# Kernel optimization log

Measured on AMD Instinct MI355X. Metric: run time of the kernel, lower is better.

Reference implementation:

```python
import jax, jax.numpy as jnp
import numpy as np

K = 20
EPS = 1e-5
SLOPE = 0.2


def setup_inputs() -> dict:
    key = jax.random.key(0)
    k1, k2 = jax.random.split(key, 2)
    B, C, N, O = 2, 64, 8192, 64
    x = jax.random.normal(k1, (B, C, N), dtype=jnp.float32)
    W = jax.random.normal(k2, (O, 2 * C), dtype=jnp.float32) * 0.05  # Conv2d 1x1, bias=False
    gamma = jnp.ones((O,), dtype=jnp.float32)
    beta = jnp.zeros((O,), dtype=jnp.float32)
    return {"x": x, "W": W, "gamma": gamma, "beta": beta}


def reference(x, W, gamma, beta):
    # x: (B, C, N)
    B, C, N = x.shape
    xt = jnp.swapaxes(x, 1, 2)  # (B, N, C)

    # --- get_GraphFeatures: KNN by negative squared euclidean distance ---
    inner = jnp.einsum('bnc,bmc->bnm', xt, xt)          # (B, N, N)
    sq = jnp.sum(xt * xt, axis=-1)                      # (B, N)
    neg_dist = 2.0 * inner - sq[:, :, None] - sq[:, None, :]
    _, idx = jax.lax.top_k(neg_dist, K)                 # (B, N, K) int32

    # gather neighbor features: (B, N, K, C)
    nbr = jax.vmap(lambda pts, i: pts[i])(xt, idx)
    center = xt[:, :, None, :]                          # (B, N, 1, C)
    # edge feature: concat(x_j - x_i, x_i) -> (B, N, K, 2C)
    edge = jnp.concatenate([nbr - center, jnp.broadcast_to(center, nbr.shape)], axis=-1)

    # --- 1x1 conv (pointwise GEMM) -> (B, O, N, K) ---
    h = jnp.einsum('bnkf,of->bonk', edge, W)

    # --- BatchNorm2d (training-mode batch stats over B, N, K per channel) ---
    mean = jnp.mean(h, axis=(0, 2, 3), keepdims=True)
    var = jnp.var(h, axis=(0, 2, 3), keepdims=True)
    h = (h - mean) * jax.lax.rsqrt(var + EPS)
    h = h * gamma[None, :, None, None] + beta[None, :, None, None]

    # --- LeakyReLU(0.2) + max over neighbors ---
    h = jnp.where(h >= 0, h, SLOPE * h)
    return jnp.max(h, axis=-1)                          # (B, O, N)
```

## Files before the change

kernel.cpp:

```cpp
#include <hip/hip_runtime.h>
#include <cfloat>

#define BB 2
#define NN 8192
#define OO 64
#define KK 20
#define QB 128
#define MS 8
#define CHUNK 1024
#define CAPQ 192
#define RB 9
#define RBS 10

using f16x8  = __attribute__((ext_vector_type(8))) _Float16;
using f32x16 = __attribute__((ext_vector_type(16))) float;
typedef unsigned long long u64;

#define XH_OFF ((size_t)0)
#define XL_OFF (XH_OFF + (size_t)BB*NN*32)
#define SQ_OFF (XL_OFF + (size_t)BB*NN*32)
#define Y1_OFF (SQ_OFF + (size_t)BB*NN)
#define Y2_OFF (Y1_OFF + (size_t)BB*NN*64)
#define TH_OFF (Y2_OFF + (size_t)BB*NN*64)
#define CN_OFF (TH_OFF + (size_t)BB*NN)
#define TL_OFF (CN_OFF + (size_t)BB*NN)
#define CA_OFF (TL_OFF + (size_t)2*BB*NN*KK)
#define IX_OFF (CA_OFF + (size_t)BB*NN*CAPQ*2)
#define HX_OFF (IX_OFF + (size_t)BB*NN*KK)
#define HN_OFF (HX_OFF + (size_t)BB*NN*64)
#define ST_OFF (HN_OFF + (size_t)BB*NN*64)

__device__ __forceinline__ size_t frag_off(int b, int tile, int t, int lane) {
    return ((((size_t)b * (NN / 32) + tile) * 4 + t) * 64 + lane) * 8;
}

__device__ __forceinline__ unsigned fmap(float f) {
    unsigned u = __float_as_uint(f);
    return (u & 0x80000000u) ? ~u : (u | 0x80000000u);
}

__device__ __forceinline__ void sort16(float* v) {
#pragma unroll
    for (int k = 2; k <= 16; k <<= 1) {
#pragma unroll
        for (int j = k >> 1; j > 0; j >>= 1) {
#pragma unroll
            for (int i = 0; i < 16; ++i) {
                int l = i ^ j;
                if (l > i) {
                    bool up = ((i & k) == 0);
                    float mn = fminf(v[i], v[l]);
                    float mx = fmaxf(v[i], v[l]);
                    v[i] = up ? mn : mx;
                    v[l] = up ? mx : mn;
                }
            }
        }
    }
}
__device__ __forceinline__ void bmerge32(float* A) {
#pragma unroll
    for (int j = 16; j > 0; j >>= 1) {
#pragma unroll
        for (int i = 0; i < 32; ++i) {
            if ((i & j) == 0) {
                float mn = fminf(A[i], A[i | j]);
                float mx = fmaxf(A[i], A[i | j]);
                A[i] = mn;
                A[i | j] = mx;
            }
        }
    }
}
__device__ __forceinline__ void merge32_16(float* A, const float* B) {
#pragma unroll
    for (int i = 16; i < 32; ++i) A[i] = fminf(A[i], B[31 - i]);
    bmerge32(A);
}
__device__ __forceinline__ void merge32_32(float* A, const float* B) {
    float t[32];
#pragma unroll
    for (int i = 0; i < 32; ++i) t[i] = fminf(A[i], B[31 - i]);
    bmerge32(t);
#pragma unroll
    for (int i = 0; i < 32; ++i) A[i] = t[i];
}

__device__ __forceinline__ void load_atile(const _Float16* __restrict__ xh,
                                           const _Float16* __restrict__ xl,
                                           int b, int ptile, int lane,
                                           f16x8* Ah, f16x8* Al) {
#pragma unroll
    for (int t = 0; t < 4; ++t) {
        size_t o = frag_off(b, ptile, t, lane);
        Ah[t] = *(const f16x8*)&xh[o];
        Al[t] = *(const f16x8*)&xl[o];
    }
}

__device__ __forceinline__ void dist_from_frags(const f16x8* Ah, const f16x8* Al,
                                                const float* sqs, int sbase, int kh,
                                                const f16x8* Qh, const f16x8* Ql,
                                                float* dv) {
    f32x16 c0, c1;
#pragma unroll
    for (int i = 0; i < 16; ++i) { c0[i] = 0.f; c1[i] = 0.f; }
#pragma unroll
    for (int t = 0; t < 4; ++t) {
        c0 = __builtin_amdgcn_mfma_f32_32x32x16_f16(Ah[t], Qh[t], c0, 0, 0, 0);
        c1 = __builtin_amdgcn_mfma_f32_32x32x16_f16(Ah[t], Ql[t], c1, 0, 0, 0);
        c1 = __builtin_amdgcn_mfma_f32_32x32x16_f16(Al[t], Qh[t], c1, 0, 0, 0);
    }
#pragma unroll
    for (int r2 = 0; r2 < 4; ++r2) {
        float4 sv = *(const float4*)&sqs[sbase + 8 * r2 + 4 * kh];
        float svv[4] = {sv.x, sv.y, sv.z, sv.w};
#pragma unroll
        for (int j = 0; j < 4; ++j) {
            int i = r2 * 4 + j;
            float d = fmaf(-2.f, c0[i], svv[j]);
            dv[i] = fmaf(-9.765625e-4f, c1[i], d);
        }
    }
}

__device__ __forceinline__ void load_qfrag(const _Float16* __restrict__ xh,
                                           const _Float16* __restrict__ xl,
                                           int b, int qbase, int lane,
                                           f16x8* Qh, f16x8* Ql) {
    const int qtile = qbase >> 5;
#pragma unroll
    for (int t = 0; t < 4; ++t) {
        size_t o = frag_off(b, qtile, t, lane);
        Qh[t] = *(const f16x8*)&xh[o];
        Ql[t] = *(const f16x8*)&xl[o];
    }
}

__global__ void __launch_bounds__(256, 2)
kA(const float* __restrict__ x, const float* __restrict__ W,
   float* __restrict__ ws) {
    __shared__ __align__(16) float w1s[32 * 64];
    __shared__ __align__(16) float w2s[32 * 64];
    __shared__ float xs[64 * 65];
    __shared__ float tb[64 * 33];
    const int bb = blockIdx.z;
    const int og = blockIdx.y;
    const int obase = og * 32;
    const int nbase = blockIdx.x * 64;
    const int tn = threadIdx.x & 63, tq = threadIdx.x >> 6;

    for (int i = threadIdx.x; i < 2048; i += 256) {
        int ol = i >> 6, c = i & 63;
        float a = W[(obase + ol) * 128 + c];
        float d = W[(obase + ol) * 128 + 64 + c];
        w1s[i] = a;
        w2s[i] = d - a;
    }
    for (int i = threadIdx.x; i < 4096; i += 256) {
        int c = i >> 6, nl = i & 63;
        xs[c * 65 + nl] = x[((size_t)bb * 64 + c) * NN + nbase + nl];
    }
    if (og == 0) {
        if (blockIdx.x == 0 && bb == 0 && threadIdx.x < 128)
            ws[ST_OFF + threadIdx.x] = 0.f;
        int gid = (bb * 128 + blockIdx.x) * 256 + threadIdx.x;
        if (gid < BB * NN) ((int*)(ws + CN_OFF))[gid] = 0;
    }
    __syncthreads();

    float xc[64];
#pragma unroll
    for (int c = 0; c < 64; ++c) xc[c] = xs[c * 65 + tn];

    if (og == 0 && tq == 0) {
        float sqv = 0.f;
#pragma unroll
        for (int c = 0; c < 64; ++c) sqv = fmaf(xc[c], xc[c], sqv);
        int n = nbase + tn;
        ws[SQ_OFF + (size_t)bb * NN + n] = sqv;
        _Float16* xh = (_Float16*)(ws + XH_OFF);
        _Float16* xl = (_Float16*)(ws + XL_OFF);
        int tile = n >> 5, r = n & 31;
#pragma unroll
        for (int t = 0; t < 4; ++t) {
#pragma unroll
            for (int kh = 0; kh < 2; ++kh) {
                f16x8 vh, vl;
#pragma unroll
                for (int j = 0; j < 8; ++j) {
                    float v = xc[t * 16 + kh * 8 + j];
                    _Float16 h = (_Float16)v;
                    vh[j] = h;
                    vl[j] = (_Float16)((v - (float)h) * 2048.f);
                }
                size_t o = frag_off(bb, tile, t, kh * 32 + r);
                *(f16x8*)&xh[o] = vh;
                *(f16x8*)&xl[o] = vl;
            }
        }
    }

    float a1v[8], a2v[8];
#pragma unroll
    for (int o2 = 0; o2 < 8; ++o2) {
        int ol = tq * 8 + o2;
        const float4* w1v = (const float4*)&w1s[ol * 64];
        const float4* w2v = (const float4*)&w2s[ol * 64];
        float a1 = 0.f, a2 = 0.f;
#pragma unroll
        for (int c4 = 0; c4 < 16; ++c4) {
            float4 v1 = w1v[c4];
            float4 v2 = w2v[c4];
            a1 = fmaf(v1.x, xc[4*c4],   a1);
            a1 = fmaf(v1.y, xc[4*c4+1], a1);
            a1 = fmaf(v1.z, xc[4*c4+2], a1);
            a1 = fmaf(v1.w, xc[4*c4+3], a1);
            a2 = fmaf(v2.x, xc[4*c4],   a2);
            a2 = fmaf(v2.y, xc[4*c4+1], a2);
            a2 = fmaf(v2.z, xc[4*c4+2], a2);
            a2 = fmaf(v2.w, xc[4*c4+3], a2);
        }
        a1v[o2] = a1;
        a2v[o2] = a2;
    }

    const int lo = threadIdx.x & 31;
    const int lp = (threadIdx.x >> 5) & 1;
#pragma unroll
    for (int o2 = 0; o2 < 8; ++o2)
        tb[tn * 33 + tq * 8 + o2] = a1v[o2];
    __syncthreads();
#pragma unroll
    for (int j = 0; j < 8; ++j) {
        int r = tq * 16 + 2 * j + lp;
        ws[Y1_OFF + ((size_t)bb * NN + nbase + r) * 64 + obase + lo] = tb[r * 33 + lo];
    }
    __syncthreads();
#pragma unroll
    for (int o2 = 0; o2 < 8; ++o2)
        tb[tn * 33 + tq * 8 + o2] = a2v[o2];
    __syncthreads();
#pragma unroll
    for (int j = 0; j < 8; ++j) {
        int r = tq * 16 + 2 * j + lp;
        ws[Y2_OFF + ((size_t)bb * NN + nbase + r) * 64 + obase + lo] = tb[r * 33 + lo];
    }
}

__global__ void __launch_bounds__(256, 3)
kT(const _Float16* __restrict__ xh, const _Float16* __restrict__ xl,
   const float* __restrict__ sq, float* __restrict__ thrL) {
    __shared__ float mrg[32 * 128];
    __shared__ __align__(16) float sqs[1024];
    const int tid  = threadIdx.x;
    const int lane = tid & 63;
    const int wv   = tid >> 6;
    const int qcol = lane & 31;
    const int kh   = lane >> 5;
    const int b     = blockIdx.y >> 1;
    const int s     = blockIdx.y & 1;
    const int qbase = blockIdx.x * 32;

    for (int i = tid; i < 1024; i += 256)
        sqs[i] = sq[(size_t)b * NN + s * 1024 + i];

    f16x8 Qh[4], Ql[4];
    load_qfrag(xh, xl, b, qbase, lane, Qh, Ql);
    __syncthreads();

    float dk[32];
#pragma unroll
    for (int i = 0; i < 32; ++i) dk[i] = FLT_MAX;

    const int p0 = s * 1024 + wv * 256;
    for (int pt = p0; pt < p0 + 256; pt += 32) {
        f16x8 Ah[4], Al[4];
        load_atile(xh, xl, b, pt >> 5, lane, Ah, Al);
        float dv[16];
        dist_from_frags(Ah, Al, sqs, pt - s * 1024, kh, Qh, Ql, dv);
        float m16 = dv[0];
#pragma unroll
        for (int i = 1; i < 16; ++i) m16 = fminf(m16, dv[i]);
        if (__any(m16 < dk[KK - 1])) {
            sort16(dv);
            merge32_16(dk, dv);
        }
    }

    {
        float B[32];
#pragma unroll
        for (int j = 0; j < 32; ++j) B[j] = __shfl(dk[j], lane | 32);
        merge32_32(dk, B);
    }
    if (kh == 0) {
#pragma unroll
        for (int j = 0; j < 32; ++j) mrg[j * 128 + wv * 32 + qcol] = dk[j];
    }
    __syncthreads();

    if (tid < 32) {
        float B[32];
#pragma unroll 1
        for (int w = 1; w < 4; ++w) {
#pragma unroll
            for (int j = 0; j < 32; ++j) B[j] = mrg[j * 128 + w * 32 + tid];
            merge32_32(dk, B);
        }
        size_t base = (((size_t)b * 2 + s) * NN + qbase + tid) * KK;
#pragma unroll
        for (int j = 0; j < KK; ++j) thrL[base + j] = dk[j];
    }
}

__global__ void kM2(const float* __restrict__ thrL, float* __restrict__ thr) {
    int gid = blockIdx.x * 256 + threadIdx.x;
    int b = gid >> 13, q = gid & (NN - 1);
    const float* A = &thrL[(((size_t)b * 2 + 0) * NN + q) * KK];
    const float* B = &thrL[(((size_t)b * 2 + 1) * NN + q) * KK];
    int ia = 0, ib = 0;
    float v = 0.f;
#pragma unroll
    for (int t = 0; t < KK; ++t) {
        float av = A[ia], bv = B[ib];
        bool ta = av <= bv;
        v = ta ? av : bv;
        ia += ta ? 1 : 0;
        ib += ta ? 0 : 1;
    }
    thr[gid] = v + fabsf(v) * 1e-6f + 1e-6f;
}

__global__ void __launch_bounds__(256, 4)
kS(const _Float16* __restrict__ xh, const _Float16* __restrict__ xl,
   const float* __restrict__ sq, const float* __restrict__ thr,
   int* __restrict__ cnt, u64* __restrict__ cand) {
    __shared__ __align__(16) char tbuf[2][8192];
    __shared__ u64 lbuf[256 * RBS];
    __shared__ __align__(16) float sqs[CHUNK];
    const int tid  = threadIdx.x;
    const int lane = tid & 63;
    const int wv   = tid >> 6;
    const int qcol = lane & 31;
    const int kh   = lane >> 5;
    const int id     = blockIdx.x;
    const int ychunk = id & 7;
    const int qt     = (id >> 3) & 63;
    const int b      = (id >> 9) & 1;
    const int qbase  = qt * QB + wv * 32;
    const int pbase0 = ychunk * CHUNK;
    const int ptile0 = pbase0 >> 5;

    auto stage = [&](int ptile, char* buf) {
        const _Float16* gh = &xh[frag_off(b, ptile, wv, lane)];
        const _Float16* gl = &xl[frag_off(b, ptile, wv, lane)];
        __builtin_amdgcn_global_load_lds(
            (const __attribute__((address_space(1))) void*)gh,
            (__attribute__((address_space(3))) void*)(buf + wv * 1024), 16, 0, 0);
        __builtin_amdgcn_global_load_lds(
            (const __attribute__((address_space(1))) void*)gl,
            (__attribute__((address_space(3))) void*)(buf + 4096 + wv * 1024), 16, 0, 0);
    };

    for (int i = tid; i < CHUNK; i += 256)
        sqs[i] = sq[(size_t)b * NN + pbase0 + i];

    f16x8 Qh[4], Ql[4];
    load_qfrag(xh, xl, b, qbase, lane, Qh, Ql);

    const size_t qidx = (size_t)b * NN + qbase + qcol;
    const float tv = thr[qidx];
    const size_t cb = qidx * CAPQ;
    int c_ = 0;

    stage(ptile0, tbuf[0]);
    __syncthreads();

    auto flushS = [&]() {
        if (c_ > 0) {
            int base = atomicAdd(&cnt[qidx], c_);
#pragma unroll 1
            for (int j = 0; j < c_; ++j) {
                int slot = base + j;
                if (slot < CAPQ) cand[cb + slot] = lbuf[tid * RBS + j];
            }
            c_ = 0;
        }
    };

#pragma unroll 1
    for (int tt = 0; tt < CHUNK / 32; ++tt) {
        if (tt + 1 < CHUNK / 32)
            stage(ptile0 + tt + 1, tbuf[(tt + 1) & 1]);

        const char* cbuf = tbuf[tt & 1];
        f16x8 Ah[4], Al[4];
#pragma unroll
        for (int t = 0; t < 4; ++t) {
            Ah[t] = *(const f16x8*)(cbuf + t * 1024 + lane * 16);
            Al[t] = *(const f16x8*)(cbuf + 4096 + t * 1024 + lane * 16);
        }
        float dv[16];
        dist_from_frags(Ah, Al, sqs, tt * 32, kh, Qh, Ql, dv);

        const int pb4 = pbase0 + tt * 32 + 4 * kh;
#pragma unroll
        for (int i = 0; i < 16; ++i) {
            float d = dv[i];
            if (d <= tv) {
                int id2 = pb4 + ((i & 3) + 8 * (i >> 2));
                lbuf[tid * RBS + c_] = ((u64)fmap(d) << 32) | (unsigned)id2;
                if (++c_ == RB) flushS();
            }
        }
        __syncthreads();
    }
    flushS();
}

__global__ void __launch_bounds__(64)
kP(const int* __restrict__ cnt, const u64* __restrict__ cand,
   int* __restrict__ idxK) {
    const int lane = threadIdx.x;
    const int qloc = lane & 31;
    const int par  = lane >> 5;
    const int q = blockIdx.x * 32 + qloc;
    int m = cnt[q];
    m = m < CAPQ ? m : CAPQ;
    const int nj = (m - par + 1) >> 1;
    u64 kk[KK];
#pragma unroll
    for (int i = 0; i < KK; ++i) kk[i] = ~0ull;

    auto insU = [&](u64 v) {
        kk[KK - 1] = v;
#pragma unroll
        for (int i = KK - 1; i > 0; --i) {
            u64 a = kk[i - 1], c = kk[i];
            bool sw = c < a;
            kk[i - 1] = sw ? c : a;
            kk[i]     = sw ? a : c;
        }
    };

    const u64* cp = &cand[(size_t)q * CAPQ + par];
#pragma unroll 1
    for (int j = 0; j < CAPQ / 2; ++j) {
        if (!__any(j < nj)) break;
        u64 v = cp[2 * j];
        if ((j < nj) && v < kk[KK - 1]) insU(v);
    }

#pragma unroll
    for (int j = 0; j < KK; ++j) {
        u64 v = __shfl(kk[j], lane | 32);
        bool ins = (par == 0) && v < kk[KK - 1];
        if (!__any(ins)) break;
        if (ins) insU(v);
    }

    if (par == 0) {
        int* op = &idxK[(size_t)q * KK];
#pragma unroll
        for (int i = 0; i < KK; ++i) op[i] = (int)(unsigned)(kk[i] & 0xffffffffu);
    }
}

__global__ void kC1(const float* __restrict__ y1, const float* __restrict__ y2,
                    const int* __restrict__ idxK, float* __restrict__ hmaxT,
                    float* __restrict__ hminT, float* __restrict__ stats) {
    __shared__ int li[32 * KK];
    __shared__ float red[256];
    __shared__ float thm[32 * 65];
    __shared__ float thn[32 * 65];
    int b = blockIdx.y;
    int o = threadIdx.x & 63;
    int nn = threadIdx.x >> 6;
    int nbase = blockIdx.x * 32;

    for (int i = threadIdx.x; i < 32 * KK; i += 256)
        li[i] = idxK[((size_t)b * NN + nbase) * KK + i];
    __syncthreads();

    float s = 0.f, ss = 0.f;
    for (int gidx = 0; gidx < 8; ++gidx) {
        int nl = gidx * 4 + nn;
        int n = nbase + nl;
        float y2v = y2[((size_t)b * NN + n) * 64 + o];
        float hm = -FLT_MAX, hn = FLT_MAX;
        const int* lin = &li[nl * KK];
#pragma unroll 4
        for (int k = 0; k < KK; ++k) {
            int j = lin[k];
            float h = y1[((size_t)b * NN + j) * 64 + o] + y2v;
            s += h;
            ss += h * h;
            hm = fmaxf(hm, h);
            hn = fminf(hn, h);
        }
        thm[nl * 65 + o] = hm;
        thn[nl * 65 + o] = hn;
    }
    __syncthreads();

    int l = threadIdx.x & 31, g = threadIdx.x >> 5;
#pragma unroll
    for (int i = 0; i < 8; ++i) {
        int o2 = g * 8 + i;
        hmaxT[((size_t)b * 64 + o2) * NN + nbase + l] = thm[l * 65 + o2];
        hminT[((size_t)b * 64 + o2) * NN + nbase + l] = thn[l * 65 + o2];
    }

    __syncthreads();
    red[threadIdx.x] = s;
    __syncthreads();
    if (threadIdx.x < 64) {
        float v = red[o] + red[64 + o] + red[128 + o] + red[192 + o];
        atomicAdd(&stats[o], v);
    }
    __syncthreads();
    red[threadIdx.x] = ss;
    __syncthreads();
    if (threadIdx.x < 64) {
        float v = red[o] + red[64 + o] + red[128 + o] + red[192 + o];
        atomicAdd(&stats[64 + o], v);
    }
}

__global__ void kC3(const float* __restrict__ hmaxT, const float* __restrict__ hminT,
                    const float* __restrict__ stats, const float* __restrict__ gamma,
                    const float* __restrict__ beta, float* __restrict__ out) {
    int o = blockIdx.x;
    int half = blockIdx.y;
    int b = blockIdx.z;
    const float c = (float)BB * NN * KK;
    float mean = stats[o] / c;
    float var = stats[64 + o] / c - mean * mean;
    float rs = rsqrtf(var + 1e-5f);
    float a = gamma[o] * rs;
    float b2 = beta[o] - a * mean;
    size_t rowb = ((size_t)b * 64 + o) * NN;
    int n0 = half * (NN / 2), n1 = n0 + NN / 2;
    for (int n = n0 + threadIdx.x; n < n1; n += 256) {
        float hm = hmaxT[rowb + n];
        float hn = hminT[rowb + n];
        float hs = (a >= 0.f) ? hm : hn;
        float v = a * hs + b2;
        v = (v >= 0.f) ? v : 0.2f * v;
        out[rowb + n] = v;
    }
}

extern "C" void kernel_launch(void* const* d_in, const int* in_sizes, int n_in,
                              void* d_out, int out_size, void* d_ws, size_t ws_size,
                              hipStream_t stream) {
    const float* x     = (const float*)d_in[0];
    const float* W     = (const float*)d_in[1];
    const float* gamma = (const float*)d_in[2];
    const float* beta  = (const float*)d_in[3];
    float* out = (float*)d_out;
    float* ws  = (float*)d_ws;

    _Float16* xh = (_Float16*)(ws + XH_OFF);
    _Float16* xl = (_Float16*)(ws + XL_OFF);
    float* sq    = ws + SQ_OFF;
    float* y1    = ws + Y1_OFF;
    float* y2    = ws + Y2_OFF;
    float* thr   = ws + TH_OFF;
    int*   cnt   = (int*)(ws + CN_OFF);
    float* thrL  = ws + TL_OFF;
    u64*   cand  = (u64*)(ws + CA_OFF);
    int*   idxK  = (int*)(ws + IX_OFF);
    float* hmaxT = ws + HX_OFF;
    float* hminT = ws + HN_OFF;
    float* stats = ws + ST_OFF;

    kA<<<dim3(NN / 64, 2, BB), 256, 0, stream>>>(x, W, ws);
    kT<<<dim3(NN / 32, 2 * BB), 256, 0, stream>>>(xh, xl, sq, thrL);
    kM2<<<dim3(BB * NN / 256), 256, 0, stream>>>(thrL, thr);
    kS<<<dim3(MS * (NN / QB) * BB), 256, 0, stream>>>(xh, xl, sq, thr, cnt, cand);
    kP<<<dim3(BB * NN / 32), 64, 0, stream>>>(cnt, cand, idxK);
    kC1<<<dim3(NN / 32, BB), 256, 0, stream>>>(y1, y2, idxK, hmaxT, hminT, stats);
    kC3<<<dim3(OO, 2, BB), 256, 0, stream>>>(hmaxT, hminT, stats, gamma, beta, out);
}
```

Before: 281.5 us.

## Parallelize candidate selection 4-way, vectorize threshold merge, batch gather loads

kM2 now loads each pair of sorted 20-element lists with float4 loads and finds the 20th smallest through a branch-free min/max formula instead of a serial merge with dependent loads. kP assigns four lanes to each query instead of two, unrolls the candidate loop by two, and combines the per-lane top-K lists with a two-level butterfly merge. kC1 issues all 20 neighbor gathers before reducing, to overlap memory latency, and gets launch bounds. The trade-off is more registers per thread and extra merge steps in kP.

```diff
diff --git a/kernel.cpp b/kernel.cpp
--- a/kernel.cpp
+++ b/kernel.cpp
@@ -317,18 +317,20 @@
 __global__ void kM2(const float* __restrict__ thrL, float* __restrict__ thr) {
     int gid = blockIdx.x * 256 + threadIdx.x;
     int b = gid >> 13, q = gid & (NN - 1);
-    const float* A = &thrL[(((size_t)b * 2 + 0) * NN + q) * KK];
-    const float* B = &thrL[(((size_t)b * 2 + 1) * NN + q) * KK];
-    int ia = 0, ib = 0;
-    float v = 0.f;
-#pragma unroll
-    for (int t = 0; t < KK; ++t) {
-        float av = A[ia], bv = B[ib];
-        bool ta = av <= bv;
-        v = ta ? av : bv;
-        ia += ta ? 1 : 0;
-        ib += ta ? 0 : 1;
-    }
+    float A[KK], Bv[KK];
+    const float4* pa = (const float4*)&thrL[(((size_t)b * 2 + 0) * NN + q) * KK];
+    const float4* pb = (const float4*)&thrL[(((size_t)b * 2 + 1) * NN + q) * KK];
+#pragma unroll
+    for (int i = 0; i < 5; ++i) {
+        float4 va = pa[i];
+        float4 vb = pb[i];
+        A[4*i] = va.x;  A[4*i+1] = va.y;  A[4*i+2] = va.z;  A[4*i+3] = va.w;
+        Bv[4*i] = vb.x; Bv[4*i+1] = vb.y; Bv[4*i+2] = vb.z; Bv[4*i+3] = vb.w;
+    }
+    float v = fminf(Bv[KK - 1], A[KK - 1]);
+#pragma unroll
+    for (int i = 1; i < KK; ++i)
+        v = fminf(v, fmaxf(A[i - 1], Bv[KK - 1 - i]));
     thr[gid] = v + fabsf(v) * 1e-6f + 1e-6f;
 }
 
@@ -419,16 +421,23 @@
     flushS();
 }
 
-__global__ void __launch_bounds__(64)
+__global__ void __launch_bounds__(256)
 kP(const int* __restrict__ cnt, const u64* __restrict__ cand,
    int* __restrict__ idxK) {
-    const int lane = threadIdx.x;
-    const int qloc = lane & 31;
-    const int par  = lane >> 5;
-    const int q = blockIdx.x * 32 + qloc;
+    const int tid  = threadIdx.x;
+    const int par  = tid & 3;
+    const int q = blockIdx.x * 64 + (tid >> 2);
     int m = cnt[q];
     m = m < CAPQ ? m : CAPQ;
-    const int nj = (m - par + 1) >> 1;
+    const int nj = (m - par + 3) >> 2;
+
+    int njW = nj;
+#pragma unroll
+    for (int s2 = 32; s2 >= 1; s2 >>= 1) {
+        int o = __shfl_xor(njW, s2);
+        njW = njW > o ? njW : o;
+    }
+
     u64 kk[KK];
 #pragma unroll
     for (int i = 0; i < KK; ++i) kk[i] = ~0ull;
@@ -446,18 +455,27 @@
 
     const u64* cp = &cand[(size_t)q * CAPQ + par];
 #pragma unroll 1
-    for (int j = 0; j < CAPQ / 2; ++j) {
-        if (!__any(j < nj)) break;
-        u64 v = cp[2 * j];
-        if ((j < nj) && v < kk[KK - 1]) insU(v);
-    }
-
-#pragma unroll
-    for (int j = 0; j < KK; ++j) {
-        u64 v = __shfl(kk[j], lane | 32);
-        bool ins = (par == 0) && v < kk[KK - 1];
-        if (!__any(ins)) break;
-        if (ins) insU(v);
+    for (int j = 0; j < njW; j += 2) {
+        u64 v0 = cp[4 * j];
+        u64 v1 = cp[4 * (j + 1)];
+        bool i0 = (j < nj) && v0 < kk[KK - 1];
+        bool i1 = (j + 1 < nj) && v1 < kk[KK - 1];
+        if (__any(i0 || i1)) {
+            if (i0) insU(v0);
+            if (i1 && v1 < kk[KK - 1]) insU(v1);
+        }
+    }
+
+#pragma unroll
+    for (int s2 = 2; s2 >= 1; s2 >>= 1) {
+        bool absorb = (par & s2) == 0;
+#pragma unroll 1
+        for (int j = 0; j < KK; ++j) {
+            u64 v = __shfl_xor(kk[j], s2);
+            bool ins = absorb && v < kk[KK - 1];
+            if (!__any(ins)) break;
+            if (ins) insU(v);
+        }
     }
 
     if (par == 0) {
@@ -467,9 +485,10 @@
     }
 }
 
-__global__ void kC1(const float* __restrict__ y1, const float* __restrict__ y2,
-                    const int* __restrict__ idxK, float* __restrict__ hmaxT,
-                    float* __restrict__ hminT, float* __restrict__ stats) {
+__global__ void __launch_bounds__(256, 2)
+kC1(const float* __restrict__ y1, const float* __restrict__ y2,
+    const int* __restrict__ idxK, float* __restrict__ hmaxT,
+    float* __restrict__ hminT, float* __restrict__ stats) {
     __shared__ int li[32 * KK];
     __shared__ float red[256];
     __shared__ float thm[32 * 65];
@@ -488,12 +507,17 @@
         int nl = gidx * 4 + nn;
         int n = nbase + nl;
         float y2v = y2[((size_t)b * NN + n) * 64 + o];
-        float hm = -FLT_MAX, hn = FLT_MAX;
         const int* lin = &li[nl * KK];
-#pragma unroll 4
+        float hv[KK];
+#pragma unroll
         for (int k = 0; k < KK; ++k) {
             int j = lin[k];
-            float h = y1[((size_t)b * NN + j) * 64 + o] + y2v;
+            hv[k] = y1[((size_t)b * NN + j) * 64 + o];
+        }
+        float hm = -FLT_MAX, hn = FLT_MAX;
+#pragma unroll
+        for (int k = 0; k < KK; ++k) {
+            float h = hv[k] + y2v;
             s += h;
             ss += h * h;
             hm = fmaxf(hm, h);
@@ -580,7 +604,7 @@
     kT<<<dim3(NN / 32, 2 * BB), 256, 0, stream>>>(xh, xl, sq, thrL);
     kM2<<<dim3(BB * NN / 256), 256, 0, stream>>>(thrL, thr);
     kS<<<dim3(MS * (NN / QB) * BB), 256, 0, stream>>>(xh, xl, sq, thr, cnt, cand);
-    kP<<<dim3(BB * NN / 32), 64, 0, stream>>>(cnt, cand, idxK);
+    kP<<<dim3(BB * NN / 64), 256, 0, stream>>>(cnt, cand, idxK);
     kC1<<<dim3(NN / 32, BB), 256, 0, stream>>>(y1, y2, idxK, hmaxT, hminT, stats);
     kC3<<<dim3(OO, 2, BB), 256, 0, stream>>>(hmaxT, hminT, stats, gamma, beta, out);
 }
```

Measured after the change: 292.7 us. 4.0% more time.
